# Performance work log

Hardware: AMD Instinct MI355X
Metric: run time of the kernel (lower is better)

The kernel has to match this reference:

```python
import jax, jax.numpy as jnp
import numpy as np
import math

B, S, D, H = 1, 4096, 1024, 16
DH = D // H  # head_dim = 64
NEG = -10000.0  # matches torch masked-fill value in source (not -inf)


def setup_inputs() -> dict:
    key = jax.random.key(0)
    ks = jax.random.split(key, 5)
    scale = 0.02
    return {
        "x": jax.random.normal(ks[0], (B, S, D), dtype=jnp.float32),
        "Wqkv_w": jax.random.normal(ks[1], (3 * D, D), dtype=jnp.float32) * scale,
        "Wqkv_b": jax.random.normal(ks[2], (3 * D,), dtype=jnp.float32) * scale,
        "out_w": jax.random.normal(ks[3], (D, D), dtype=jnp.float32) * scale,
        "out_b": jax.random.normal(ks[4], (D,), dtype=jnp.float32) * scale,
    }


def reference(x, Wqkv_w, Wqkv_b, out_w, out_b):
    # QKV projection: (B,S,D) @ (D,3D) + b -> (B,S,3,H,DH)
    qkv = jnp.einsum('bsd,ed->bse', x, Wqkv_w) + Wqkv_b
    qkv = qkv.reshape(B, S, 3, H, DH)
    q, k, v = qkv[:, :, 0], qkv[:, :, 1], qkv[:, :, 2]  # each (B,S,H,DH)
    softmax_scale = 1.0 / math.sqrt(DH)
    # scores: (B,H,T,S)
    scores = jnp.einsum('bthd,bshd->bhts', q, k * softmax_scale)
    # causal additive mask with -10000 above diagonal (faithful to source)
    causal_mask = jnp.triu(jnp.full((S, S), NEG, dtype=scores.dtype), k=1)
    scores = scores + causal_mask
    attention = jax.nn.softmax(scores, axis=-1)
    context = jnp.einsum('bhts,bshd->bthd', attention, v)  # (B,T,H,DH)
    context = context.reshape(B, S, D)
    out = jnp.einsum('bsd,ed->bse', context, out_w) + out_b
    return out
```

## Files before the change

### kernel.cpp

```cpp
#include <hip/hip_runtime.h>
#include <hip/hip_bf16.h>

using f32x4  = __attribute__((ext_vector_type(4))) float;
using f32x16 = __attribute__((ext_vector_type(16))) float;
using bf16x8 = __attribute__((ext_vector_type(8))) __bf16;
using u16x8  = __attribute__((ext_vector_type(8))) unsigned short;
using u32x4  = __attribute__((ext_vector_type(4))) unsigned int;

#define DEV __device__ __forceinline__

constexpr int S_  = 4096;
constexpr int D_  = 1024;
constexpr int KD  = 1024;

constexpr size_t XB_OFF   = 0;
constexpr size_t WQKV_OFF = 8388608;
constexpr size_t WOUT_OFF = 14680064;
constexpr size_t QB_OFF   = 16777216;
constexpr size_t KB_OFF   = 25165824;
constexpr size_t VT_OFF   = 33554432;
constexpr size_t CTX_OFF  = 41943040;

DEV unsigned short f2bf(float f) {
  __hip_bfloat16 h = __float2bfloat16(f);
  return __builtin_bit_cast(unsigned short, h);
}

DEV void gl_lds16(const void* g, void* l) {
  __builtin_amdgcn_global_load_lds(
      (const __attribute__((address_space(1))) void*)g,
      (__attribute__((address_space(3))) void*)l, 16, 0, 0);
}

DEV f32x4 mfma16(bf16x8 a, bf16x8 b, f32x4 c) {
  return __builtin_amdgcn_mfma_f32_16x16x32_bf16(a, b, c, 0, 0, 0);
}
DEV f32x16 mfma32(bf16x8 a, bf16x8 b, f32x16 c) {
  return __builtin_amdgcn_mfma_f32_32x32x16_bf16(a, b, c, 0, 0, 0);
}
DEV unsigned cvtpk(float lo, float hi) {
  unsigned r;
  asm("v_cvt_pk_bf16_f32 %0, %1, %2" : "=v"(r) : "v"(lo), "v"(hi));
  return r;
}
DEV float exp2_fast(float x) {
  float r;
  asm("v_exp_f32 %0, %1" : "=v"(r) : "v"(x));
  return r;
}
DEV void pl32(unsigned& a, unsigned& b) {
  asm("v_permlane32_swap_b32 %0, %1" : "+v"(a), "+v"(b));
}
DEV float xhalf_add(float x) {
  float y;
  asm("v_mov_b32 %0, %1" : "=v"(y) : "v"(x));
  unsigned a = __builtin_bit_cast(unsigned, x), b = __builtin_bit_cast(unsigned, y);
  pl32(a, b);
  return __builtin_bit_cast(float, a) + __builtin_bit_cast(float, b);
}

__global__ void cvt_all_k(const float* __restrict__ x,
                          const float* __restrict__ wq,
                          const float* __restrict__ wo,
                          unsigned short* __restrict__ xb,
                          unsigned short* __restrict__ wqb,
                          unsigned short* __restrict__ wob) {
  for (int u = blockIdx.x * 256 + threadIdx.x; u < 1048576; u += 2048 * 256) {
    const float* s; unsigned short* d; int off;
    if (u < 524288)      { s = x;  d = xb;  off = u; }
    else if (u < 917504) { s = wq; d = wqb; off = u - 524288; }
    else                 { s = wo; d = wob; off = u - 917504; }
    const float4* s4 = (const float4*)s;
    float4 a = s4[2 * off], b = s4[2 * off + 1];
    u16x8 o;
    o[0] = f2bf(a.x); o[1] = f2bf(a.y); o[2] = f2bf(a.z); o[3] = f2bf(a.w);
    o[4] = f2bf(b.x); o[5] = f2bf(b.y); o[6] = f2bf(b.z); o[7] = f2bf(b.w);
    ((u16x8*)d)[off] = o;
  }
}

__global__ __launch_bounds__(256)
void gemm_qkv_k(const unsigned short* __restrict__ A,
                const unsigned short* __restrict__ Bt,
                const float* __restrict__ bias,
                unsigned short* __restrict__ qb,
                unsigned short* __restrict__ kb,
                unsigned short* __restrict__ vt) {
  __shared__ unsigned short As[2][4096];
  __shared__ unsigned short Bs[2][4096];
  const int t = threadIdx.x;
  const int w = t >> 6, l = t & 63;
  const int lr = l & 15, lg = l >> 4, lk = lg * 8;
  const int m0 = blockIdx.y * 128, n0 = blockIdx.x * 128;
  const int wm = (w >> 1) * 64, wn = (w & 1) * 64;

  f32x4 acc[4][4] = {};

  const int srow = t >> 2;
  const int scolb = (t & 3) << 4;
  const char* Ag = (const char*)A + (size_t)(m0 + srow) * (KD * 2) + scolb;
  const char* Bg = (const char*)Bt + (size_t)(n0 + srow) * (KD * 2) + scolb;

  auto stage = [&](int buf, int kt) {
    const char* ak = Ag + kt * 64;
    const char* bk = Bg + kt * 64;
    char* AsB = (char*)&As[buf][0];
    char* BsB = (char*)&Bs[buf][0];
    gl_lds16(ak,                 AsB + t * 16);
    gl_lds16(ak + 64 * (KD * 2), AsB + 4096 + t * 16);
    gl_lds16(bk,                 BsB + t * 16);
    gl_lds16(bk + 64 * (KD * 2), BsB + 4096 + t * 16);
  };

  stage(0, 0);
  for (int kt = 0; kt < KD / 32; ++kt) {
    __syncthreads();
    if (kt + 1 < KD / 32) stage((kt + 1) & 1, kt + 1);
    const int buf = kt & 1;

    bf16x8 a[4], b[4];
#pragma unroll
    for (int mi = 0; mi < 4; ++mi)
      a[mi] = *(const bf16x8*)&As[buf][(wm + mi * 16 + lr) * 32 + lk];
#pragma unroll
    for (int ni = 0; ni < 4; ++ni)
      b[ni] = *(const bf16x8*)&Bs[buf][(wn + ni * 16 + lr) * 32 + lk];
#pragma unroll
    for (int mi = 0; mi < 4; ++mi)
#pragma unroll
      for (int ni = 0; ni < 4; ++ni)
        acc[mi][ni] = mfma16(a[mi], b[ni], acc[mi][ni]);
  }

  const int r0 = lg * 4;
  const int which = n0 >> 10;
  const float kscale = 0.125f * 1.44269504088896f;
#pragma unroll
  for (int mi = 0; mi < 4; ++mi) {
    const int sbase = m0 + wm + mi * 16 + r0;
#pragma unroll
    for (int ni = 0; ni < 4; ++ni) {
      const int e = n0 + wn + ni * 16 + lr;
      const float bv = bias[e];
      const int h = (e & 1023) >> 6, dd = e & 63;
#pragma unroll
      for (int r = 0; r < 4; ++r) {
        const float v = acc[mi][ni][r] + bv;
        const int sr = sbase + r;
        if (which == 0)      qb[((size_t)(h * S_ + sr)) * 64 + dd] = f2bf(v);
        else if (which == 1) kb[((size_t)(h * S_ + sr)) * 64 + dd] = f2bf(v * kscale);
        else                 vt[((size_t)(h * 64 + dd)) * S_ + sr] = f2bf(v);
      }
    }
  }
}

__global__ __launch_bounds__(256)
void gemm_proj_k(const unsigned short* __restrict__ A,
                 const unsigned short* __restrict__ Bt,
                 const float* __restrict__ bias,
                 float* __restrict__ outf) {
  __shared__ unsigned short As[2][4096];
  __shared__ unsigned short Bs[2][2048];
  const int t = threadIdx.x;
  const int w = t >> 6, l = t & 63;
  const int lr = l & 15, lg = l >> 4, lk = lg * 8;
  const int m0 = blockIdx.y * 128, n0 = blockIdx.x * 64;
  const int wm = (w >> 1) * 64, wn = (w & 1) * 32;

  f32x4 acc[4][2] = {};

  const int srow = t >> 2;
  const int scolb = (t & 3) << 4;
  const char* Ag = (const char*)A + (size_t)(m0 + srow) * (KD * 2) + scolb;
  const char* Bg = (const char*)Bt + (size_t)(n0 + (t >> 2)) * (KD * 2) + scolb;

  auto stage = [&](int buf, int kt) {
    const char* ak = Ag + kt * 64;
    char* AsB = (char*)&As[buf][0];
    gl_lds16(ak,                 AsB + t * 16);
    gl_lds16(ak + 64 * (KD * 2), AsB + 4096 + t * 16);
    gl_lds16(Bg + kt * 64, (char*)&Bs[buf][0] + t * 16);
  };

  stage(0, 0);
  for (int kt = 0; kt < KD / 32; ++kt) {
    __syncthreads();
    if (kt + 1 < KD / 32) stage((kt + 1) & 1, kt + 1);
    const int buf = kt & 1;

    bf16x8 a[4], b[2];
#pragma unroll
    for (int mi = 0; mi < 4; ++mi)
      a[mi] = *(const bf16x8*)&As[buf][(wm + mi * 16 + lr) * 32 + lk];
#pragma unroll
    for (int ni = 0; ni < 2; ++ni)
      b[ni] = *(const bf16x8*)&Bs[buf][(wn + ni * 16 + lr) * 32 + lk];
#pragma unroll
    for (int mi = 0; mi < 4; ++mi)
#pragma unroll
      for (int ni = 0; ni < 2; ++ni)
        acc[mi][ni] = mfma16(a[mi], b[ni], acc[mi][ni]);
  }

  const int r0 = lg * 4;
#pragma unroll
  for (int mi = 0; mi < 4; ++mi) {
    const int sbase = m0 + wm + mi * 16 + r0;
#pragma unroll
    for (int ni = 0; ni < 2; ++ni) {
      const int e = n0 + wn + ni * 16 + lr;
      const float bv = bias[e];
#pragma unroll
      for (int r = 0; r < 4; ++r)
        outf[(size_t)(sbase + r) * D_ + e] = acc[mi][ni][r] + bv;
    }
  }
}

__global__ __launch_bounds__(512, 2)
void attn_k(const unsigned short* __restrict__ Qb,
            const unsigned short* __restrict__ Kb,
            const unsigned short* __restrict__ Vt,
            unsigned short* __restrict__ ctx) {
  __shared__ char smem[65536];

  const int t = threadIdx.x;
  const int w8 = t >> 6;
  const int g  = w8 >> 2;
  const int w  = w8 & 3;
  const int l = t & 63, lq = l & 31, hi = l >> 5;
  const int b = blockIdx.x + (blockIdx.y << 4);
  const int h = ((b & 7) << 1) | ((b >> 3) & 1);
  const int pairIdx = b >> 4;

  const int sg = t >> 8;
  const int ts = t & 255;
  const int srow = ts >> 3;
  const int ssw  = ((ts & 7) << 4) ^ ((srow & 7) << 4);
  const char* Kg0 = (const char*)Kb + (size_t)(h * S_) * 128;
  const char* Vg0 = (const char*)Vt + (size_t)(h * 64) * (size_t)(S_ * 2);

  for (int task = 0; task < 2; ++task) {
    const int bi = task == 0 ? (31 - pairIdx) : pairIdx;
    const int q0 = bi * 128;
    const int qrow = q0 + w * 32 + lq;
    const int qwmin = q0 + w * 32, qwmax = qwmin + 31;
    const int niter = bi + 1;

    const unsigned short* Qr = Qb + ((size_t)(h * S_ + qrow)) * 64;
    bf16x8 qf[4];
#pragma unroll
    for (int d0 = 0; d0 < 4; ++d0)
      qf[d0] = *(const bf16x8*)(Qr + d0 * 16 + hi * 8);

    f32x16 cacc[2] = {};
    float lsum = 0.f;

    auto stage = [&](int buf, int tl) {
      const int kv0 = tl * 64;
      char* kd = smem + sg * 16384 + buf * 8192;
      const char* Kg = Kg0 + (size_t)kv0 * 128;
      gl_lds16(Kg + (size_t)srow * 128 + ssw,        kd + ts * 16);
      gl_lds16(Kg + (size_t)(32 + srow) * 128 + ssw, kd + 4096 + ts * 16);
      char* vd = smem + 32768 + sg * 16384 + buf * 8192;
      const char* Vg = Vg0 + (size_t)kv0 * 2;
      gl_lds16(Vg + (size_t)srow * (S_ * 2) + ssw,        vd + ts * 16);
      gl_lds16(Vg + (size_t)(32 + srow) * (S_ * 2) + ssw, vd + 4096 + ts * 16);
    };

    int cur = 0;
    stage(0, sg * niter);

    for (int it = 0; it < niter; ++it) {
      __syncthreads();
      if (it + 1 < niter) stage(cur ^ 1, it + 1 + sg * niter);
      const char* Kt = smem + g * 16384 + cur * 8192;
      const char* Vl = smem + 32768 + g * 16384 + cur * 8192;
      const int tl = it + g * niter;

      if (tl * 64 + 63 <= qwmin) {
        f32x16 st0, st1;
#pragma unroll
        for (int r = 0; r < 16; ++r) { st0[r] = -8.0f; st1[r] = -8.0f; }
        const char* kb0 = Kt + lq * 128;
        const char* kb1 = Kt + (32 + lq) * 128;
        const int ksw = (lq & 7) << 4;
        __builtin_amdgcn_s_setprio(1);
#pragma unroll
        for (int d0 = 0; d0 < 4; ++d0) {
          bf16x8 kf0 = *(const bf16x8*)(kb0 + ((d0 * 32 + hi * 16) ^ ksw));
          bf16x8 kf1 = *(const bf16x8*)(kb1 + ((d0 * 32 + hi * 16) ^ ksw));
          st0 = mfma32(kf0, qf[d0], st0);
          st1 = mfma32(kf1, qf[d0], st1);
        }
        __builtin_amdgcn_s_setprio(0);

#pragma unroll
        for (int r = 0; r < 16; ++r) { st0[r] = exp2_fast(st0[r]); st1[r] = exp2_fast(st1[r]); }
        float a0 = (st0[0] + st0[1]) + (st0[2] + st0[3]);
        float a1 = (st0[4] + st0[5]) + (st0[6] + st0[7]);
        float a2 = (st0[8] + st0[9]) + (st0[10] + st0[11]);
        float a3 = (st0[12] + st0[13]) + (st0[14] + st0[15]);
        float b0 = (st1[0] + st1[1]) + (st1[2] + st1[3]);
        float b1 = (st1[4] + st1[5]) + (st1[6] + st1[7]);
        float b2 = (st1[8] + st1[9]) + (st1[10] + st1[11]);
        float b3 = (st1[12] + st1[13]) + (st1[14] + st1[15]);
        lsum += xhalf_add(((a0 + a1) + (a2 + a3)) + ((b0 + b1) + (b2 + b3)));

        unsigned x0 = cvtpk(st0[0], st0[1]),   x1 = cvtpk(st0[2], st0[3]);
        unsigned y0 = cvtpk(st0[4], st0[5]),   y1 = cvtpk(st0[6], st0[7]);
        pl32(x0, y0); pl32(x1, y1);
        u32x4 f00 = {x0, x1, y0, y1};
        bf16x8 pf00 = __builtin_bit_cast(bf16x8, f00);
        unsigned x2 = cvtpk(st0[8], st0[9]),   x3 = cvtpk(st0[10], st0[11]);
        unsigned y2 = cvtpk(st0[12], st0[13]), y3 = cvtpk(st0[14], st0[15]);
        pl32(x2, y2); pl32(x3, y3);
        u32x4 f01 = {x2, x3, y2, y3};
        bf16x8 pf01 = __builtin_bit_cast(bf16x8, f01);
        unsigned u0 = cvtpk(st1[0], st1[1]),   u1 = cvtpk(st1[2], st1[3]);
        unsigned v0w = cvtpk(st1[4], st1[5]),  v1w = cvtpk(st1[6], st1[7]);
        pl32(u0, v0w); pl32(u1, v1w);
        u32x4 f10 = {u0, u1, v0w, v1w};
        bf16x8 pf10 = __builtin_bit_cast(bf16x8, f10);
        unsigned u2 = cvtpk(st1[8], st1[9]),   u3 = cvtpk(st1[10], st1[11]);
        unsigned v2w = cvtpk(st1[12], st1[13]), v3w = cvtpk(st1[14], st1[15]);
        pl32(u2, v2w); pl32(u3, v3w);
        u32x4 f11 = {u2, u3, v2w, v3w};
        bf16x8 pf11 = __builtin_bit_cast(bf16x8, f11);

        __builtin_amdgcn_s_setprio(1);
#pragma unroll
        for (int db = 0; db < 2; ++db) {
          const int dr = db * 32 + lq;
          const char* vbase = Vl + dr * 128;
          const int vsw = (dr & 7) << 4;
          bf16x8 va = *(const bf16x8*)(vbase + ((hi * 16) ^ vsw));
          bf16x8 vb = *(const bf16x8*)(vbase + ((32 + hi * 16) ^ vsw));
          bf16x8 vc = *(const bf16x8*)(vbase + ((64 + hi * 16) ^ vsw));
          bf16x8 vd = *(const bf16x8*)(vbase + ((96 + hi * 16) ^ vsw));
          cacc[db] = mfma32(va, pf00, cacc[db]);
          cacc[db] = mfma32(vb, pf01, cacc[db]);
          cacc[db] = mfma32(vc, pf10, cacc[db]);
          cacc[db] = mfma32(vd, pf11, cacc[db]);
        }
        __builtin_amdgcn_s_setprio(0);
      } else {
#pragma unroll
        for (int kvh = 0; kvh < 2; ++kvh) {
          const int kv0s = tl * 64 + kvh * 32;
          if (kv0s > qwmax) continue;

          f32x16 st;
#pragma unroll
          for (int r = 0; r < 16; ++r) st[r] = -8.0f;
          const int kr = kvh * 32 + lq;
          const char* kbase = Kt + kr * 128;
          const int ksw = (kr & 7) << 4;
#pragma unroll
          for (int d0 = 0; d0 < 4; ++d0) {
            bf16x8 kf = *(const bf16x8*)(kbase + ((d0 * 32 + hi * 16) ^ ksw));
            st = mfma32(kf, qf[d0], st);
          }

          if (kv0s + 31 > qwmin) {
#pragma unroll
            for (int r = 0; r < 16; ++r) {
              const int kvg = kv0s + (r & 3) + 8 * (r >> 2) + 4 * hi;
              if (kvg > qrow) st[r] = -INFINITY;
            }
          }

#pragma unroll
          for (int r = 0; r < 16; ++r) st[r] = exp2_fast(st[r]);
          float a0 = (st[0] + st[1]) + (st[2] + st[3]);
          float a1 = (st[4] + st[5]) + (st[6] + st[7]);
          float a2 = (st[8] + st[9]) + (st[10] + st[11]);
          float a3 = (st[12] + st[13]) + (st[14] + st[15]);
          lsum += xhalf_add((a0 + a1) + (a2 + a3));

          unsigned x0 = cvtpk(st[0], st[1]),   x1 = cvtpk(st[2], st[3]);
          unsigned y0 = cvtpk(st[4], st[5]),   y1 = cvtpk(st[6], st[7]);
          pl32(x0, y0); pl32(x1, y1);
          u32x4 f0 = {x0, x1, y0, y1};
          bf16x8 pf0 = __builtin_bit_cast(bf16x8, f0);
          unsigned x2 = cvtpk(st[8], st[9]),   x3 = cvtpk(st[10], st[11]);
          unsigned y2 = cvtpk(st[12], st[13]), y3 = cvtpk(st[14], st[15]);
          pl32(x2, y2); pl32(x3, y3);
          u32x4 f1 = {x2, x3, y2, y3};
          bf16x8 pf1 = __builtin_bit_cast(bf16x8, f1);

#pragma unroll
          for (int db = 0; db < 2; ++db) {
            const int dr = db * 32 + lq;
            const char* vbase = Vl + dr * 128;
            const int vsw = (dr & 7) << 4;
            bf16x8 v0 = *(const bf16x8*)(vbase + ((kvh * 64 + hi * 16) ^ vsw));
            bf16x8 v1 = *(const bf16x8*)(vbase + ((kvh * 64 + 32 + hi * 16) ^ vsw));
            cacc[db] = mfma32(v0, pf0, cacc[db]);
            cacc[db] = mfma32(v1, pf1, cacc[db]);
          }
        }
      }
      cur ^= 1;
    }

    __syncthreads();
    float* slot = (float*)smem + (size_t)(w * 64 + l) * 36;
    if (g == 1) {
      slot[0] = lsum;
#pragma unroll
      for (int j = 0; j < 16; ++j) { slot[1 + j] = cacc[0][j]; slot[17 + j] = cacc[1][j]; }
    }
    __syncthreads();
    if (g == 0) {
      const float inv = 1.0f / (lsum + slot[0]);
      unsigned short* base = ctx + (size_t)qrow * D_ + h * 64;
#pragma unroll
      for (int db = 0; db < 2; ++db)
#pragma unroll
        for (int r = 0; r < 16; r += 2) {
          const float o0 = (cacc[db][r]     + slot[1 + db * 16 + r])     * inv;
          const float o1 = (cacc[db][r + 1] + slot[1 + db * 16 + r + 1]) * inv;
          const unsigned wv = cvtpk(o0, o1);
          const int d = (r & 3) + 8 * (r >> 2) + 4 * hi + 32 * db;
          *(unsigned*)(base + d) = wv;
        }
    }
    __syncthreads();
  }
}

extern "C" void kernel_launch(void* const* d_in, const int* in_sizes, int n_in,
                              void* d_out, int out_size, void* d_ws, size_t ws_size,
                              hipStream_t stream) {
  const float* x      = (const float*)d_in[0];
  const float* Wqkv_w = (const float*)d_in[1];
  const float* Wqkv_b = (const float*)d_in[2];
  const float* out_w  = (const float*)d_in[3];
  const float* out_b  = (const float*)d_in[4];
  float* out = (float*)d_out;
  char* ws = (char*)d_ws;

  unsigned short* xb    = (unsigned short*)(ws + XB_OFF);
  unsigned short* wqkvb = (unsigned short*)(ws + WQKV_OFF);
  unsigned short* woutb = (unsigned short*)(ws + WOUT_OFF);
  unsigned short* Qb    = (unsigned short*)(ws + QB_OFF);
  unsigned short* Kb    = (unsigned short*)(ws + KB_OFF);
  unsigned short* Vt    = (unsigned short*)(ws + VT_OFF);
  unsigned short* ctx   = (unsigned short*)(ws + CTX_OFF);

  cvt_all_k<<<2048, 256, 0, stream>>>(x, Wqkv_w, out_w, xb, wqkvb, woutb);

  gemm_qkv_k<<<dim3(24, 32), 256, 0, stream>>>(xb, wqkvb, Wqkv_b, Qb, Kb, Vt);

  attn_k<<<dim3(16, 16), 512, 0, stream>>>(Qb, Kb, Vt, ctx);

  gemm_proj_k<<<dim3(16, 32), 256, 0, stream>>>(ctx, woutb, out_b, out);
}
```

Before: 131.4 us.

## Split attention into one query block per workgroup and vectorize V-transpose stores

The attention kernel no longer loops over a pair of query blocks (one long, one short) inside each workgroup. It launches twice as many workgroups, each handling a single query block, and orders them so the longest causal blocks are scheduled first. The launch bounds now request four workgroups per CU, which caps register use per thread and may cause spills. Separately, the QKV GEMM epilogue writes the transposed V output as packed 4-element stores along the sequence dimension instead of scalar stores.

```diff
diff --git a/kernel.cpp b/kernel.cpp
--- a/kernel.cpp
+++ b/kernel.cpp
@@ -4,6 +4,7 @@
 using f32x4  = __attribute__((ext_vector_type(4))) float;
 using f32x16 = __attribute__((ext_vector_type(16))) float;
 using bf16x8 = __attribute__((ext_vector_type(8))) __bf16;
+using u16x4  = __attribute__((ext_vector_type(4))) unsigned short;
 using u16x8  = __attribute__((ext_vector_type(8))) unsigned short;
 using u32x4  = __attribute__((ext_vector_type(4))) unsigned int;
 
@@ -118,38 +119,54 @@
     if (kt + 1 < KD / 32) stage((kt + 1) & 1, kt + 1);
     const int buf = kt & 1;
 
-    bf16x8 a[4], b[4];
+    bf16x8 a[4], bb[4];
 #pragma unroll
     for (int mi = 0; mi < 4; ++mi)
       a[mi] = *(const bf16x8*)&As[buf][(wm + mi * 16 + lr) * 32 + lk];
 #pragma unroll
     for (int ni = 0; ni < 4; ++ni)
-      b[ni] = *(const bf16x8*)&Bs[buf][(wn + ni * 16 + lr) * 32 + lk];
+      bb[ni] = *(const bf16x8*)&Bs[buf][(wn + ni * 16 + lr) * 32 + lk];
 #pragma unroll
     for (int mi = 0; mi < 4; ++mi)
 #pragma unroll
       for (int ni = 0; ni < 4; ++ni)
-        acc[mi][ni] = mfma16(a[mi], b[ni], acc[mi][ni]);
+        acc[mi][ni] = mfma16(a[mi], bb[ni], acc[mi][ni]);
   }
 
   const int r0 = lg * 4;
   const int which = n0 >> 10;
   const float kscale = 0.125f * 1.44269504088896f;
-#pragma unroll
-  for (int mi = 0; mi < 4; ++mi) {
-    const int sbase = m0 + wm + mi * 16 + r0;
-#pragma unroll
-    for (int ni = 0; ni < 4; ++ni) {
-      const int e = n0 + wn + ni * 16 + lr;
-      const float bv = bias[e];
-      const int h = (e & 1023) >> 6, dd = e & 63;
-#pragma unroll
-      for (int r = 0; r < 4; ++r) {
-        const float v = acc[mi][ni][r] + bv;
-        const int sr = sbase + r;
-        if (which == 0)      qb[((size_t)(h * S_ + sr)) * 64 + dd] = f2bf(v);
-        else if (which == 1) kb[((size_t)(h * S_ + sr)) * 64 + dd] = f2bf(v * kscale);
-        else                 vt[((size_t)(h * 64 + dd)) * S_ + sr] = f2bf(v);
+  if (which == 2) {
+#pragma unroll
+    for (int mi = 0; mi < 4; ++mi) {
+      const int sbase = m0 + wm + mi * 16 + r0;
+#pragma unroll
+      for (int ni = 0; ni < 4; ++ni) {
+        const int e = n0 + wn + ni * 16 + lr;
+        const float bv = bias[e];
+        const int h = (e & 1023) >> 6, dd = e & 63;
+        u16x4 pk;
+#pragma unroll
+        for (int r = 0; r < 4; ++r) pk[r] = f2bf(acc[mi][ni][r] + bv);
+        *(u16x4*)(vt + (size_t)(h * 64 + dd) * S_ + sbase) = pk;
+      }
+    }
+  } else {
+#pragma unroll
+    for (int mi = 0; mi < 4; ++mi) {
+      const int sbase = m0 + wm + mi * 16 + r0;
+#pragma unroll
+      for (int ni = 0; ni < 4; ++ni) {
+        const int e = n0 + wn + ni * 16 + lr;
+        const float bv = bias[e];
+        const int h = (e & 1023) >> 6, dd = e & 63;
+#pragma unroll
+        for (int r = 0; r < 4; ++r) {
+          const float v = acc[mi][ni][r] + bv;
+          const int sr = sbase + r;
+          if (which == 0) qb[((size_t)(h * S_ + sr)) * 64 + dd] = f2bf(v);
+          else            kb[((size_t)(h * S_ + sr)) * 64 + dd] = f2bf(v * kscale);
+        }
       }
     }
   }
@@ -189,18 +206,18 @@
     if (kt + 1 < KD / 32) stage((kt + 1) & 1, kt + 1);
     const int buf = kt & 1;
 
-    bf16x8 a[4], b[2];
+    bf16x8 a[4], bb[2];
 #pragma unroll
     for (int mi = 0; mi < 4; ++mi)
       a[mi] = *(const bf16x8*)&As[buf][(wm + mi * 16 + lr) * 32 + lk];
 #pragma unroll
     for (int ni = 0; ni < 2; ++ni)
-      b[ni] = *(const bf16x8*)&Bs[buf][(wn + ni * 16 + lr) * 32 + lk];
+      bb[ni] = *(const bf16x8*)&Bs[buf][(wn + ni * 16 + lr) * 32 + lk];
 #pragma unroll
     for (int mi = 0; mi < 4; ++mi)
 #pragma unroll
       for (int ni = 0; ni < 2; ++ni)
-        acc[mi][ni] = mfma16(a[mi], b[ni], acc[mi][ni]);
+        acc[mi][ni] = mfma16(a[mi], bb[ni], acc[mi][ni]);
   }
 
   const int r0 = lg * 4;
@@ -218,7 +235,7 @@
   }
 }
 
-__global__ __launch_bounds__(512, 2)
+__global__ __launch_bounds__(512, 4)
 void attn_k(const unsigned short* __restrict__ Qb,
             const unsigned short* __restrict__ Kb,
             const unsigned short* __restrict__ Vt,
@@ -230,9 +247,10 @@
   const int g  = w8 >> 2;
   const int w  = w8 & 3;
   const int l = t & 63, lq = l & 31, hi = l >> 5;
-  const int b = blockIdx.x + (blockIdx.y << 4);
+  const int b = blockIdx.x + (blockIdx.y << 5);
   const int h = ((b & 7) << 1) | ((b >> 3) & 1);
-  const int pairIdx = b >> 4;
+  const int qi = b >> 4;
+  const int bi = qi < 16 ? (31 - qi) : (qi - 16);
 
   const int sg = t >> 8;
   const int ts = t & 255;
@@ -241,193 +259,189 @@
   const char* Kg0 = (const char*)Kb + (size_t)(h * S_) * 128;
   const char* Vg0 = (const char*)Vt + (size_t)(h * 64) * (size_t)(S_ * 2);
 
-  for (int task = 0; task < 2; ++task) {
-    const int bi = task == 0 ? (31 - pairIdx) : pairIdx;
-    const int q0 = bi * 128;
-    const int qrow = q0 + w * 32 + lq;
-    const int qwmin = q0 + w * 32, qwmax = qwmin + 31;
-    const int niter = bi + 1;
-
-    const unsigned short* Qr = Qb + ((size_t)(h * S_ + qrow)) * 64;
-    bf16x8 qf[4];
-#pragma unroll
-    for (int d0 = 0; d0 < 4; ++d0)
-      qf[d0] = *(const bf16x8*)(Qr + d0 * 16 + hi * 8);
-
-    f32x16 cacc[2] = {};
-    float lsum = 0.f;
-
-    auto stage = [&](int buf, int tl) {
-      const int kv0 = tl * 64;
-      char* kd = smem + sg * 16384 + buf * 8192;
-      const char* Kg = Kg0 + (size_t)kv0 * 128;
-      gl_lds16(Kg + (size_t)srow * 128 + ssw,        kd + ts * 16);
-      gl_lds16(Kg + (size_t)(32 + srow) * 128 + ssw, kd + 4096 + ts * 16);
-      char* vd = smem + 32768 + sg * 16384 + buf * 8192;
-      const char* Vg = Vg0 + (size_t)kv0 * 2;
-      gl_lds16(Vg + (size_t)srow * (S_ * 2) + ssw,        vd + ts * 16);
-      gl_lds16(Vg + (size_t)(32 + srow) * (S_ * 2) + ssw, vd + 4096 + ts * 16);
-    };
-
-    int cur = 0;
-    stage(0, sg * niter);
-
-    for (int it = 0; it < niter; ++it) {
-      __syncthreads();
-      if (it + 1 < niter) stage(cur ^ 1, it + 1 + sg * niter);
-      const char* Kt = smem + g * 16384 + cur * 8192;
-      const char* Vl = smem + 32768 + g * 16384 + cur * 8192;
-      const int tl = it + g * niter;
-
-      if (tl * 64 + 63 <= qwmin) {
-        f32x16 st0, st1;
-#pragma unroll
-        for (int r = 0; r < 16; ++r) { st0[r] = -8.0f; st1[r] = -8.0f; }
-        const char* kb0 = Kt + lq * 128;
-        const char* kb1 = Kt + (32 + lq) * 128;
-        const int ksw = (lq & 7) << 4;
-        __builtin_amdgcn_s_setprio(1);
+  const int q0 = bi * 128;
+  const int qrow = q0 + w * 32 + lq;
+  const int qwmin = q0 + w * 32, qwmax = qwmin + 31;
+  const int niter = bi + 1;
+
+  const unsigned short* Qr = Qb + ((size_t)(h * S_ + qrow)) * 64;
+  bf16x8 qf[4];
+#pragma unroll
+  for (int d0 = 0; d0 < 4; ++d0)
+    qf[d0] = *(const bf16x8*)(Qr + d0 * 16 + hi * 8);
+
+  f32x16 cacc[2] = {};
+  float lsum = 0.f;
+
+  auto stage = [&](int buf, int tl) {
+    const int kv0 = tl * 64;
+    char* kd = smem + sg * 16384 + buf * 8192;
+    const char* Kg = Kg0 + (size_t)kv0 * 128;
+    gl_lds16(Kg + (size_t)srow * 128 + ssw,        kd + ts * 16);
+    gl_lds16(Kg + (size_t)(32 + srow) * 128 + ssw, kd + 4096 + ts * 16);
+    char* vd = smem + 32768 + sg * 16384 + buf * 8192;
+    const char* Vg = Vg0 + (size_t)kv0 * 2;
+    gl_lds16(Vg + (size_t)srow * (S_ * 2) + ssw,        vd + ts * 16);
+    gl_lds16(Vg + (size_t)(32 + srow) * (S_ * 2) + ssw, vd + 4096 + ts * 16);
+  };
+
+  int cur = 0;
+  stage(0, sg * niter);
+
+  for (int it = 0; it < niter; ++it) {
+    __syncthreads();
+    if (it + 1 < niter) stage(cur ^ 1, it + 1 + sg * niter);
+    const char* Kt = smem + g * 16384 + cur * 8192;
+    const char* Vl = smem + 32768 + g * 16384 + cur * 8192;
+    const int tl = it + g * niter;
+
+    if (tl * 64 + 63 <= qwmin) {
+      f32x16 st0, st1;
+#pragma unroll
+      for (int r = 0; r < 16; ++r) { st0[r] = -8.0f; st1[r] = -8.0f; }
+      const char* kb0 = Kt + lq * 128;
+      const char* kb1 = Kt + (32 + lq) * 128;
+      const int ksw = (lq & 7) << 4;
+      __builtin_amdgcn_s_setprio(1);
+#pragma unroll
+      for (int d0 = 0; d0 < 4; ++d0) {
+        bf16x8 kf0 = *(const bf16x8*)(kb0 + ((d0 * 32 + hi * 16) ^ ksw));
+        bf16x8 kf1 = *(const bf16x8*)(kb1 + ((d0 * 32 + hi * 16) ^ ksw));
+        st0 = mfma32(kf0, qf[d0], st0);
+        st1 = mfma32(kf1, qf[d0], st1);
+      }
+      __builtin_amdgcn_s_setprio(0);
+
+#pragma unroll
+      for (int r = 0; r < 16; ++r) { st0[r] = exp2_fast(st0[r]); st1[r] = exp2_fast(st1[r]); }
+      float a0 = (st0[0] + st0[1]) + (st0[2] + st0[3]);
+      float a1 = (st0[4] + st0[5]) + (st0[6] + st0[7]);
+      float a2 = (st0[8] + st0[9]) + (st0[10] + st0[11]);
+      float a3 = (st0[12] + st0[13]) + (st0[14] + st0[15]);
+      float b0 = (st1[0] + st1[1]) + (st1[2] + st1[3]);
+      float b1 = (st1[4] + st1[5]) + (st1[6] + st1[7]);
+      float b2 = (st1[8] + st1[9]) + (st1[10] + st1[11]);
+      float b3 = (st1[12] + st1[13]) + (st1[14] + st1[15]);
+      lsum += xhalf_add(((a0 + a1) + (a2 + a3)) + ((b0 + b1) + (b2 + b3)));
+
+      unsigned x0 = cvtpk(st0[0], st0[1]),   x1 = cvtpk(st0[2], st0[3]);
+      unsigned y0 = cvtpk(st0[4], st0[5]),   y1 = cvtpk(st0[6], st0[7]);
+      pl32(x0, y0); pl32(x1, y1);
+      u32x4 f00 = {x0, x1, y0, y1};
+      bf16x8 pf00 = __builtin_bit_cast(bf16x8, f00);
+      unsigned x2 = cvtpk(st0[8], st0[9]),   x3 = cvtpk(st0[10], st0[11]);
+      unsigned y2 = cvtpk(st0[12], st0[13]), y3 = cvtpk(st0[14], st0[15]);
+      pl32(x2, y2); pl32(x3, y3);
+      u32x4 f01 = {x2, x3, y2, y3};
+      bf16x8 pf01 = __builtin_bit_cast(bf16x8, f01);
+      unsigned u0 = cvtpk(st1[0], st1[1]),    u1 = cvtpk(st1[2], st1[3]);
+      unsigned v0w = cvtpk(st1[4], st1[5]),   v1w = cvtpk(st1[6], st1[7]);
+      pl32(u0, v0w); pl32(u1, v1w);
+      u32x4 f10 = {u0, u1, v0w, v1w};
+      bf16x8 pf10 = __builtin_bit_cast(bf16x8, f10);
+      unsigned u2 = cvtpk(st1[8], st1[9]),    u3 = cvtpk(st1[10], st1[11]);
+      unsigned v2w = cvtpk(st1[12], st1[13]), v3w = cvtpk(st1[14], st1[15]);
+      pl32(u2, v2w); pl32(u3, v3w);
+      u32x4 f11 = {u2, u3, v2w, v3w};
+      bf16x8 pf11 = __builtin_bit_cast(bf16x8, f11);
+
+      __builtin_amdgcn_s_setprio(1);
+#pragma unroll
+      for (int db = 0; db < 2; ++db) {
+        const int dr = db * 32 + lq;
+        const char* vbase = Vl + dr * 128;
+        const int vsw = (dr & 7) << 4;
+        bf16x8 va = *(const bf16x8*)(vbase + ((hi * 16) ^ vsw));
+        bf16x8 vb = *(const bf16x8*)(vbase + ((32 + hi * 16) ^ vsw));
+        bf16x8 vc = *(const bf16x8*)(vbase + ((64 + hi * 16) ^ vsw));
+        bf16x8 vd = *(const bf16x8*)(vbase + ((96 + hi * 16) ^ vsw));
+        cacc[db] = mfma32(va, pf00, cacc[db]);
+        cacc[db] = mfma32(vb, pf01, cacc[db]);
+        cacc[db] = mfma32(vc, pf10, cacc[db]);
+        cacc[db] = mfma32(vd, pf11, cacc[db]);
+      }
+      __builtin_amdgcn_s_setprio(0);
+    } else {
+#pragma unroll
+      for (int kvh = 0; kvh < 2; ++kvh) {
+        const int kv0s = tl * 64 + kvh * 32;
+        if (kv0s > qwmax) continue;
+
+        f32x16 st;
+#pragma unroll
+        for (int r = 0; r < 16; ++r) st[r] = -8.0f;
+        const int kr = kvh * 32 + lq;
+        const char* kbase = Kt + kr * 128;
+        const int ksw = (kr & 7) << 4;
 #pragma unroll
         for (int d0 = 0; d0 < 4; ++d0) {
-          bf16x8 kf0 = *(const bf16x8*)(kb0 + ((d0 * 32 + hi * 16) ^ ksw));
-          bf16x8 kf1 = *(const bf16x8*)(kb1 + ((d0 * 32 + hi * 16) ^ ksw));
-          st0 = mfma32(kf0, qf[d0], st0);
-          st1 = mfma32(kf1, qf[d0], st1);
+          bf16x8 kf = *(const bf16x8*)(kbase + ((d0 * 32 + hi * 16) ^ ksw));
+          st = mfma32(kf, qf[d0], st);
         }
-        __builtin_amdgcn_s_setprio(0);
-
-#pragma unroll
-        for (int r = 0; r < 16; ++r) { st0[r] = exp2_fast(st0[r]); st1[r] = exp2_fast(st1[r]); }
-        float a0 = (st0[0] + st0[1]) + (st0[2] + st0[3]);
-        float a1 = (st0[4] + st0[5]) + (st0[6] + st0[7]);
-        float a2 = (st0[8] + st0[9]) + (st0[10] + st0[11]);
-        float a3 = (st0[12] + st0[13]) + (st0[14] + st0[15]);
-        float b0 = (st1[0] + st1[1]) + (st1[2] + st1[3]);
-        float b1 = (st1[4] + st1[5]) + (st1[6] + st1[7]);
-        float b2 = (st1[8] + st1[9]) + (st1[10] + st1[11]);
-        float b3 = (st1[12] + st1[13]) + (st1[14] + st1[15]);
-        lsum += xhalf_add(((a0 + a1) + (a2 + a3)) + ((b0 + b1) + (b2 + b3)));
-
-        unsigned x0 = cvtpk(st0[0], st0[1]),   x1 = cvtpk(st0[2], st0[3]);
-        unsigned y0 = cvtpk(st0[4], st0[5]),   y1 = cvtpk(st0[6], st0[7]);
+
+        if (kv0s + 31 > qwmin) {
+#pragma unroll
+          for (int r = 0; r < 16; ++r) {
+            const int kvg = kv0s + (r & 3) + 8 * (r >> 2) + 4 * hi;
+            if (kvg > qrow) st[r] = -INFINITY;
+          }
+        }
+
+#pragma unroll
+        for (int r = 0; r < 16; ++r) st[r] = exp2_fast(st[r]);
+        float a0 = (st[0] + st[1]) + (st[2] + st[3]);
+        float a1 = (st[4] + st[5]) + (st[6] + st[7]);
+        float a2 = (st[8] + st[9]) + (st[10] + st[11]);
+        float a3 = (st[12] + st[13]) + (st[14] + st[15]);
+        lsum += xhalf_add((a0 + a1) + (a2 + a3));
+
+        unsigned x0 = cvtpk(st[0], st[1]),   x1 = cvtpk(st[2], st[3]);
+        unsigned y0 = cvtpk(st[4], st[5]),   y1 = cvtpk(st[6], st[7]);
         pl32(x0, y0); pl32(x1, y1);
-        u32x4 f00 = {x0, x1, y0, y1};
-        bf16x8 pf00 = __builtin_bit_cast(bf16x8, f00);
-        unsigned x2 = cvtpk(st0[8], st0[9]),   x3 = cvtpk(st0[10], st0[11]);
-        unsigned y2 = cvtpk(st0[12], st0[13]), y3 = cvtpk(st0[14], st0[15]);
+        u32x4 f0 = {x0, x1, y0, y1};
+        bf16x8 pf0 = __builtin_bit_cast(bf16x8, f0);
+        unsigned x2 = cvtpk(st[8], st[9]),   x3 = cvtpk(st[10], st[11]);
+        unsigned y2 = cvtpk(st[12], st[13]), y3 = cvtpk(st[14], st[15]);
         pl32(x2, y2); pl32(x3, y3);
-        u32x4 f01 = {x2, x3, y2, y3};
-        bf16x8 pf01 = __builtin_bit_cast(bf16x8, f01);
-        unsigned u0 = cvtpk(st1[0], st1[1]),   u1 = cvtpk(st1[2], st1[3]);
-        unsigned v0w = cvtpk(st1[4], st1[5]),  v1w = cvtpk(st1[6], st1[7]);
-        pl32(u0, v0w); pl32(u1, v1w);
-        u32x4 f10 = {u0, u1, v0w, v1w};
-        bf16x8 pf10 = __builtin_bit_cast(bf16x8, f10);
-        unsigned u2 = cvtpk(st1[8], st1[9]),   u3 = cvtpk(st1[10], st1[11]);
-        unsigned v2w = cvtpk(st1[12], st1[13]), v3w = cvtpk(st1[14], st1[15]);
-        pl32(u2, v2w); pl32(u3, v3w);
-        u32x4 f11 = {u2, u3, v2w, v3w};
-        bf16x8 pf11 = __builtin_bit_cast(bf16x8, f11);
-
-        __builtin_amdgcn_s_setprio(1);
+        u32x4 f1 = {x2, x3, y2, y3};
+        bf16x8 pf1 = __builtin_bit_cast(bf16x8, f1);
+
 #pragma unroll
         for (int db = 0; db < 2; ++db) {
           const int dr = db * 32 + lq;
           const char* vbase = Vl + dr * 128;
           const int vsw = (dr & 7) << 4;
-          bf16x8 va = *(const bf16x8*)(vbase + ((hi * 16) ^ vsw));
-          bf16x8 vb = *(const bf16x8*)(vbase + ((32 + hi * 16) ^ vsw));
-          bf16x8 vc = *(const bf16x8*)(vbase + ((64 + hi * 16) ^ vsw));
-          bf16x8 vd = *(const bf16x8*)(vbase + ((96 + hi * 16) ^ vsw));
-          cacc[db] = mfma32(va, pf00, cacc[db]);
-          cacc[db] = mfma32(vb, pf01, cacc[db]);
-          cacc[db] = mfma32(vc, pf10, cacc[db]);
-          cacc[db] = mfma32(vd, pf11, cacc[db]);
+          bf16x8 v0 = *(const bf16x8*)(vbase + ((kvh * 64 + hi * 16) ^ vsw));
+          bf16x8 v1 = *(const bf16x8*)(vbase + ((kvh * 64 + 32 + hi * 16) ^ vsw));
+          cacc[db] = mfma32(v0, pf0, cacc[db]);
+          cacc[db] = mfma32(v1, pf1, cacc[db]);
         }
-        __builtin_amdgcn_s_setprio(0);
-      } else {
-#pragma unroll
-        for (int kvh = 0; kvh < 2; ++kvh) {
-          const int kv0s = tl * 64 + kvh * 32;
-          if (kv0s > qwmax) continue;
-
-          f32x16 st;
-#pragma unroll
-          for (int r = 0; r < 16; ++r) st[r] = -8.0f;
-          const int kr = kvh * 32 + lq;
-          const char* kbase = Kt + kr * 128;
-          const int ksw = (kr & 7) << 4;
-#pragma unroll
-          for (int d0 = 0; d0 < 4; ++d0) {
-            bf16x8 kf = *(const bf16x8*)(kbase + ((d0 * 32 + hi * 16) ^ ksw));
-            st = mfma32(kf, qf[d0], st);
-          }
-
-          if (kv0s + 31 > qwmin) {
-#pragma unroll
-            for (int r = 0; r < 16; ++r) {
-              const int kvg = kv0s + (r & 3) + 8 * (r >> 2) + 4 * hi;
-              if (kvg > qrow) st[r] = -INFINITY;
-            }
-          }
-
-#pragma unroll
-          for (int r = 0; r < 16; ++r) st[r] = exp2_fast(st[r]);
-          float a0 = (st[0] + st[1]) + (st[2] + st[3]);
-          float a1 = (st[4] + st[5]) + (st[6] + st[7]);
-          float a2 = (st[8] + st[9]) + (st[10] + st[11]);
-          float a3 = (st[12] + st[13]) + (st[14] + st[15]);
-          lsum += xhalf_add((a0 + a1) + (a2 + a3));
-
-          unsigned x0 = cvtpk(st[0], st[1]),   x1 = cvtpk(st[2], st[3]);
-          unsigned y0 = cvtpk(st[4], st[5]),   y1 = cvtpk(st[6], st[7]);
-          pl32(x0, y0); pl32(x1, y1);
-          u32x4 f0 = {x0, x1, y0, y1};
-          bf16x8 pf0 = __builtin_bit_cast(bf16x8, f0);
-          unsigned x2 = cvtpk(st[8], st[9]),   x3 = cvtpk(st[10], st[11]);
-          unsigned y2 = cvtpk(st[12], st[13]), y3 = cvtpk(st[14], st[15]);
-          pl32(x2, y2); pl32(x3, y3);
-          u32x4 f1 = {x2, x3, y2, y3};
-          bf16x8 pf1 = __builtin_bit_cast(bf16x8, f1);
-
-#pragma unroll
-          for (int db = 0; db < 2; ++db) {
-            const int dr = db * 32 + lq;
-            const char* vbase = Vl + dr * 128;
-            const int vsw = (dr & 7) << 4;
-            bf16x8 v0 = *(const bf16x8*)(vbase + ((kvh * 64 + hi * 16) ^ vsw));
-            bf16x8 v1 = *(const bf16x8*)(vbase + ((kvh * 64 + 32 + hi * 16) ^ vsw));
-            cacc[db] = mfma32(v0, pf0, cacc[db]);
-            cacc[db] = mfma32(v1, pf1, cacc[db]);
-          }
-        }
-      }
-      cur ^= 1;
+      }
     }
-
-    __syncthreads();
-    float* slot = (float*)smem + (size_t)(w * 64 + l) * 36;
-    if (g == 1) {
-      slot[0] = lsum;
-#pragma unroll
-      for (int j = 0; j < 16; ++j) { slot[1 + j] = cacc[0][j]; slot[17 + j] = cacc[1][j]; }
-    }
-    __syncthreads();
-    if (g == 0) {
-      const float inv = 1.0f / (lsum + slot[0]);
-      unsigned short* base = ctx + (size_t)qrow * D_ + h * 64;
-#pragma unroll
-      for (int db = 0; db < 2; ++db)
-#pragma unroll
-        for (int r = 0; r < 16; r += 2) {
-          const float o0 = (cacc[db][r]     + slot[1 + db * 16 + r])     * inv;
-          const float o1 = (cacc[db][r + 1] + slot[1 + db * 16 + r + 1]) * inv;
-          const unsigned wv = cvtpk(o0, o1);
-          const int d = (r & 3) + 8 * (r >> 2) + 4 * hi + 32 * db;
-          *(unsigned*)(base + d) = wv;
-        }
-    }
-    __syncthreads();
+    cur ^= 1;
+  }
+
+  __syncthreads();
+  float* slot = (float*)smem + (size_t)(w * 64 + l) * 36;
+  if (g == 1) {
+    slot[0] = lsum;
+#pragma unroll
+    for (int j = 0; j < 16; ++j) { slot[1 + j] = cacc[0][j]; slot[17 + j] = cacc[1][j]; }
+  }
+  __syncthreads();
+  if (g == 0) {
+    const float inv = 1.0f / (lsum + slot[0]);
+    unsigned short* base = ctx + (size_t)qrow * D_ + h * 64;
+#pragma unroll
+    for (int db = 0; db < 2; ++db)
+#pragma unroll
+      for (int r = 0; r < 16; r += 2) {
+        const float o0 = (cacc[db][r]     + slot[1 + db * 16 + r])     * inv;
+        const float o1 = (cacc[db][r + 1] + slot[1 + db * 16 + r + 1]) * inv;
+        const unsigned wv = cvtpk(o0, o1);
+        const int d = (r & 3) + 8 * (r >> 2) + 4 * hi + 32 * db;
+        *(unsigned*)(base + d) = wv;
+      }
   }
 }
 
@@ -454,7 +468,7 @@
 
   gemm_qkv_k<<<dim3(24, 32), 256, 0, stream>>>(xb, wqkvb, Wqkv_b, Qb, Kb, Vt);
 
-  attn_k<<<dim3(16, 16), 512, 0, stream>>>(Qb, Kb, Vt, ctx);
+  attn_k<<<dim3(32, 16), 512, 0, stream>>>(Qb, Kb, Vt, ctx);
 
   gemm_proj_k<<<dim3(16, 32), 256, 0, stream>>>(ctx, woutb, out_b, out);
 }
```

New measurement: 134.1 us. +2.1%, slower.
